# Performance work log

Measured on AMD Instinct MI355X. Metric: run time of the kernel, lower is better.

## Reference

```python
import jax, jax.numpy as jnp
import numpy as np

B, C, H, W = 2, 128, 64, 64


def setup_inputs() -> dict:
    key = jax.random.key(0)
    ks = jax.random.split(key, 16)
    s = 1.0 / np.sqrt(C)
    d = {
        "x": jax.random.normal(ks[0], (B, C, H, W), jnp.float32),
        "y": jax.random.normal(ks[1], (B, C, H, W), jnp.float32),
    }
    names = ["qr", "qi", "kr", "ki", "vr", "vi"]
    for i, n in enumerate(names):
        d["W" + n] = jax.random.normal(ks[2 + 2 * i], (C, C), jnp.float32) * s
        d["b" + n] = jax.random.normal(ks[3 + 2 * i], (C,), jnp.float32) * s
    return d


def _lin(t, Wt, bt):
    # t: [b, n, c]; torch Linear: t @ W^T + b
    return jnp.einsum("bnc,dc->bnd", t, Wt) + bt


def reference(x, y, Wqr, bqr, Wqi, bqi, Wkr, bkr, Wki, bki, Wvr, bvr, Wvi, bvi):
    b, c, h, w = x.shape
    xf = jnp.fft.fft2(x)  # over last two axes (h, w)
    yf = jnp.fft.fft2(y)
    # b c h w -> b (h w) c
    def flat(t):
        return t.transpose(0, 2, 3, 1).reshape(b, h * w, c)
    xr, xi = flat(xf.real), flat(xf.imag)
    yr, yi = flat(yf.real), flat(yf.imag)

    Qr = _lin(xr, Wqr, bqr) - _lin(xi, Wqi, bqi)
    Qi = _lin(xi, Wqr, bqr) + _lin(xr, Wqi, bqi)
    Kr = _lin(yr, Wkr, bkr) - _lin(yi, Wki, bki)
    Ki = _lin(yi, Wkr, bkr) + _lin(yr, Wki, bki)
    Vr = _lin(yr, Wvr, bvr) - _lin(yi, Wvi, bvi)
    Vi = _lin(yi, Wvr, bvr) + _lin(yr, Wvi, bvi)

    sr = jnp.einsum("bnc,bmc->bnm", Qr, Kr) - jnp.einsum("bnc,bmc->bnm", Qi, Ki)
    si = jnp.einsum("bnc,bmc->bnm", Qr, Ki) + jnp.einsum("bnc,bmc->bnm", Qi, Kr)
    scores = jnp.sqrt(sr * sr + si * si + 1e-8)
    attn = jax.nn.softmax(scores, axis=-1)

    out_r = jnp.einsum("bnm,bmc->bnc", attn, Vr)
    out_i = jnp.einsum("bnm,bmc->bnc", attn, Vi)
    out_c = jax.lax.complex(out_r, out_i)
    # b (h w) c -> b c h w
    out_c = out_c.reshape(b, h, w, c).transpose(0, 3, 1, 2)
    return jnp.fft.ifft2(out_c).real
```

## Files before the change

kernel.cpp:

```cpp
#include <hip/hip_runtime.h>
#include <math.h>


#define PI2 6.283185307179586f

typedef __attribute__((ext_vector_type(8))) short short8;
typedef __attribute__((ext_vector_type(4))) float f32x4;

#define MFMA16(A,B,C) __builtin_amdgcn_mfma_f32_16x16x32_bf16((A),(B),(C),0,0,0)

__device__ inline unsigned short f2bf(float x){
  union{float f; unsigned int u;} a; a.f = x;
  unsigned int r = (a.u + 0x7fffu + ((a.u>>16)&1u)) >> 16;
  return (unsigned short)r;
}
__device__ inline float bf2f(unsigned short h){
  union{unsigned int u; float f;} a; a.u = ((unsigned int)h)<<16; return a.f;
}
__device__ inline short8 neg8(short8 x){
  union{short8 v; unsigned int u[4];} a; a.v = x;
  a.u[0]^=0x80008000u; a.u[1]^=0x80008000u; a.u[2]^=0x80008000u; a.u[3]^=0x80008000u;
  return a.v;
}
__device__ inline void gload_lds16(const void* g, void* lds){
  __builtin_amdgcn_global_load_lds((const __attribute__((address_space(1))) unsigned int*)g,
                                   (__attribute__((address_space(3))) unsigned int*)lds,
                                   16, 0, 0);
}

__global__ __launch_bounds__(256) void dft2_fwd_kernel(
    const float* __restrict__ x, const float* __restrict__ y,
    float* __restrict__ xr, float* __restrict__ xi,
    float* __restrict__ yr, float* __restrict__ yi)
{
  __shared__ float Xs[4096];
  __shared__ float Tr[4096], Ti[4096];
  __shared__ float twc[64], tws[64];
  int blk = blockIdx.x;
  const float* src; float *outr, *outi;
  int plane;
  if (blk < 256) { src = x; outr = xr; outi = xi; plane = blk; }
  else           { src = y; outr = yr; outi = yi; plane = blk - 256; }
  int b = plane >> 7, c = plane & 127;
  int t = threadIdx.x;
  if (t < 64) {
    float ang = -PI2 * (float)t / 64.0f;
    twc[t] = cosf(ang); tws[t] = sinf(ang);
  }
  const float* p = src + ((size_t)plane << 12);
  for (int i = t; i < 4096; i += 256) Xs[i] = p[i];
  __syncthreads();
  for (int j = 0; j < 16; j++) {
    int o = t + 256 * j; int h = o >> 6, wp = o & 63;
    float ar = 0.f, ai = 0.f;
    for (int w = 0; w < 64; w++) {
      int k = (w * wp) & 63;
      float v = Xs[h * 64 + w];
      ar = fmaf(v, twc[k], ar);
      ai = fmaf(v, tws[k], ai);
    }
    Tr[h * 64 + wp] = ar; Ti[h * 64 + wp] = ai;
  }
  __syncthreads();
  size_t ob = ((size_t)b * 4096) * 128 + c;
  for (int j = 0; j < 16; j++) {
    int o = t + 256 * j; int hp = o >> 6, wp = o & 63;
    float ar = 0.f, ai = 0.f;
    for (int h = 0; h < 64; h++) {
      int k = (h * hp) & 63;
      float cr = twc[k], ci = tws[k];
      float tr = Tr[h * 64 + wp], ti = Ti[h * 64 + wp];
      ar += tr * cr - ti * ci;
      ai += tr * ci + ti * cr;
    }
    int n = (hp << 6) + wp;
    outr[ob + (size_t)n * 128] = ar;
    outi[ob + (size_t)n * 128] = ai;
  }
}

__global__ __launch_bounds__(256) void proj_kernel(
    const float* __restrict__ xr, const float* __restrict__ xi,
    const float* __restrict__ yr, const float* __restrict__ yi,
    const float* __restrict__ Wqr, const float* __restrict__ bqr,
    const float* __restrict__ Wqi, const float* __restrict__ bqi,
    const float* __restrict__ Wkr, const float* __restrict__ bkr,
    const float* __restrict__ Wki, const float* __restrict__ bki,
    const float* __restrict__ Wvr, const float* __restrict__ bvr,
    const float* __restrict__ Wvi, const float* __restrict__ bvi,
    unsigned short* __restrict__ FQ, unsigned short* __restrict__ FK,
    unsigned short* __restrict__ FV)
{
  __shared__ float Asr[64 * 33], Asi[64 * 33], Wsr[128 * 33], Wsi[128 * 33];
  int nt = blockIdx.x, lin = blockIdx.y, b = blockIdx.z;
  const float *ar, *ai, *Wr, *Wi, *br_, *bi_;
  unsigned short* F;
  if (lin == 0)      { ar = xr; ai = xi; Wr = Wqr; Wi = Wqi; br_ = bqr; bi_ = bqi; F = FQ; }
  else if (lin == 1) { ar = yr; ai = yi; Wr = Wkr; Wi = Wki; br_ = bkr; bi_ = bki; F = FK; }
  else               { ar = yr; ai = yi; Wr = Wvr; Wi = Wvi; br_ = bvr; bi_ = bvi; F = FV; }
  int t = threadIdx.x; int td = t & 15, tn = t >> 4;
  int n0 = nt * 64;
  size_t abase = (size_t)b * 4096 * 128 + (size_t)n0 * 128;
  const size_t PS = (size_t)2 * 4096 * 128;
  float accr[4][8] = {}, acci[4][8] = {};
  for (int kk = 0; kk < 4; kk++) {
    __syncthreads();
    for (int idx = t; idx < 64 * 32; idx += 256) {
      int r = idx >> 5, ccol = idx & 31;
      Asr[r * 33 + ccol] = ar[abase + (size_t)r * 128 + kk * 32 + ccol];
      Asi[r * 33 + ccol] = ai[abase + (size_t)r * 128 + kk * 32 + ccol];
    }
    for (int idx = t; idx < 128 * 32; idx += 256) {
      int r = idx >> 5, ccol = idx & 31;
      Wsr[r * 33 + ccol] = Wr[(size_t)r * 128 + kk * 32 + ccol];
      Wsi[r * 33 + ccol] = Wi[(size_t)r * 128 + kk * 32 + ccol];
    }
    __syncthreads();
    for (int k = 0; k < 32; k++) {
      float a_r[4], a_i[4], w_r[8], w_i[8];
      #pragma unroll
      for (int i = 0; i < 4; i++) {
        a_r[i] = Asr[(tn * 4 + i) * 33 + k];
        a_i[i] = Asi[(tn * 4 + i) * 33 + k];
      }
      #pragma unroll
      for (int jj = 0; jj < 8; jj++) {
        w_r[jj] = Wsr[(td + 16 * jj) * 33 + k];
        w_i[jj] = Wsi[(td + 16 * jj) * 33 + k];
      }
      #pragma unroll
      for (int i = 0; i < 4; i++)
        #pragma unroll
        for (int jj = 0; jj < 8; jj++) {
          accr[i][jj] += a_r[i] * w_r[jj] - a_i[i] * w_i[jj];
          acci[i][jj] += a_i[i] * w_r[jj] + a_r[i] * w_i[jj];
        }
    }
  }
  for (int jj = 0; jj < 8; jj++) {
    int d = td + 16 * jj;
    float brd = br_[d], bid = bi_[d];
    #pragma unroll
    for (int i = 0; i < 4; i++) {
      int n = n0 + tn * 4 + i;
      float cr = accr[i][jj] + (brd - bid);
      float ci = acci[i][jj] + (brd + bid);
      size_t base = ((size_t)b * 4096 + n) * 128 + d;
      if (lin <= 1) {
        unsigned short rh = f2bf(cr); unsigned short rl = f2bf(cr - bf2f(rh));
        unsigned short ih = f2bf(ci); unsigned short il = f2bf(ci - bf2f(ih));
        F[0 * PS + base] = rh;
        F[1 * PS + base] = rl;
        F[2 * PS + base] = ih;
        F[3 * PS + base] = il;
      } else {
        F[0 * PS + base] = f2bf(cr);
        F[1 * PS + base] = f2bf(ci);
      }
    }
  }
}

__global__ __launch_bounds__(256) void qpack_kernel(
    const unsigned short* __restrict__ F, unsigned short* __restrict__ Qpk)
{
  int blk = blockIdx.x;
  int b = blk >> 8, tq = blk & 255;
  int t = threadIdx.x;
  #pragma unroll
  for (int k = 0; k < 4; k++) {
    int idx = t + 256 * k;
    int l = idx & 63, s = (idx >> 6) & 3, a = idx >> 8;
    int n = tq * 16 + (l & 15);
    int c0 = 32 * s + 8 * (l >> 4);
    const short8 v = *(const short8*)(F + (((size_t)(a * 2 + b) * 4096 + n) * 128 + c0));
    *(short8*)(Qpk + (((size_t)((b * 256 + tq) * 16 + a * 4 + s)) * 64 + l) * 8) = v;
  }
}

__global__ __launch_bounds__(256) void kpack_kernel(
    const unsigned short* __restrict__ F, unsigned short* __restrict__ Kpk)
{
  int blk = blockIdx.x;
  int b = blk >> 6, mt = blk & 63;
  int t = threadIdx.x;
  size_t obase = (size_t)blk * 4096;
  #pragma unroll
  for (int k = 0; k < 16; k++) {
    int idx = t + 256 * k;
    int l = idx & 63, s = (idx >> 6) & 3, tml = (idx >> 8) & 3, a = idx >> 10;
    int n = mt * 64 + tml * 16 + (l & 15);
    int c0 = 32 * s + 8 * (l >> 4);
    const short8 v = *(const short8*)(F + (((size_t)(a * 2 + b) * 4096 + n) * 128 + c0));
    *(short8*)(Kpk + (obase + idx) * 8) = v;
  }
}

__global__ __launch_bounds__(256) void vpack_kernel(
    const unsigned short* __restrict__ F, unsigned short* __restrict__ Vpk)
{
  __shared__ unsigned short Vs[2 * 32 * 128];
  int blk = blockIdx.x;
  int b = blk >> 7, sm = blk & 127;
  int t = threadIdx.x;
  const size_t PS = (size_t)2 * 4096 * 128;
  #pragma unroll
  for (int p = 0; p < 2; p++) {
    #pragma unroll
    for (int k = 0; k < 2; k++) {
      int idx8 = t + 256 * k;
      int nn = idx8 >> 4, d0 = (idx8 & 15) * 8;
      const short8 v = *(const short8*)(F + p * PS + ((size_t)(b * 4096 + sm * 32 + nn)) * 128 + d0);
      *(short8*)(Vs + (p * 32 + nn) * 128 + d0) = v;
    }
  }
  __syncthreads();
  size_t obase = (size_t)blk * 1024;
  #pragma unroll
  for (int k = 0; k < 4; k++) {
    int idx = t + 256 * k;
    int lv = idx & 63, tc = idx >> 6;
    int vh = tc >> 3;
    int d = (tc & 7) * 16 + (lv & 15);
    int nb = (lv >> 4) * 8;
    short8 v;
    #pragma unroll
    for (int j = 0; j < 8; j++)
      v[j] = (short)Vs[(vh * 32 + nb + j) * 128 + d];
    *(short8*)(Vpk + (obase + idx) * 8) = v;
  }
}

__global__ __launch_bounds__(512, 1) void attn_mfma_kernel(
    const short* __restrict__ Qpk, const short* __restrict__ Kpk,
    const short* __restrict__ Vpk,
    float* __restrict__ Or_, float* __restrict__ Oi_)
{
  __shared__ __align__(16) short Klds[2][32768];
  __shared__ __align__(16) short Pfrag[2 * 16 * 72];
  __shared__ __align__(16) float rmax[2][16][4];
  __shared__ __align__(16) float escs[2][16];

  const int bi = blockIdx.x;
  const int xg = bi & 7;
  const int b = xg >> 2;
  const int qt = (bi >> 3) * 4 + (xg & 3);
  const int t = threadIdx.x;
  const int w = t >> 6, l = t & 63;
  const int qg = w & 1, ms = w >> 1;
  const int g = l >> 4, c = l & 15;

  const short8* Qp8 = (const short8*)Qpk;
  const int tq = qt * 2 + qg;
  short8 Qf[4][4];
  #pragma unroll
  for (int a = 0; a < 4; a++)
    #pragma unroll
    for (int s = 0; s < 4; s++)
      Qf[a][s] = Qp8[((size_t)((b * 256 + tq) * 16 + a * 4 + s)) * 64 + l];

  f32x4 O[4], Oe;
  #pragma unroll
  for (int nt = 0; nt < 4; nt++) O[nt] = (f32x4){0.f, 0.f, 0.f, 0.f};
  Oe = (f32x4){0.f, 0.f, 0.f, 0.f};
  float Mq = -3e38f;
  short8 Vreg[2][4];
  const short b1 = (short)0x3F80;
  const short8 ones = {b1, b1, b1, b1, b1, b1, b1, b1};

  const char* Kg = (const char*)Kpk;
  {
    const char* gsrc = Kg + ((size_t)(b * 64) << 16);
    char* lb = (char*)&Klds[0][0];
    #pragma unroll
    for (int i2 = 0; i2 < 8; i2++) {
      int ch = w + 8 * i2;
      gload_lds16(gsrc + ch * 1024 + l * 16, lb + ch * 1024);
    }
  }
  const short8* Vp8 = (const short8*)Vpk;
  f32x4 s0;

  for (int mt = 0; mt < 64; mt++) {
    const int cur = mt & 1;
    __syncthreads();
    if (mt + 1 < 64) {
      const char* gsrc = Kg + ((size_t)(b * 64 + mt + 1) << 16);
      char* lb = (char*)&Klds[cur ^ 1][0];
      #pragma unroll
      for (int i2 = 0; i2 < 8; i2++) {
        int ch = w + 8 * i2;
        gload_lds16(gsrc + ch * 1024 + l * 16, lb + ch * 1024);
      }
    }
    if (mt > 0) {
      f32x4 ev = *(const f32x4*)&escs[qg][4 * g];
      #pragma unroll
      for (int r = 0; r < 4; r++) {
        #pragma unroll
        for (int nt = 0; nt < 4; nt++) O[nt][r] *= ev[r];
        Oe[r] *= ev[r];
      }
      #pragma unroll
      for (int ks = 0; ks < 2; ks++) {
        short8 Pa = *(const short8*)&Pfrag[(qg * 16 + c) * 72 + 32 * ks + 8 * g];
        #pragma unroll
        for (int nt = 0; nt < 4; nt++)
          O[nt] = MFMA16(Pa, Vreg[ks][nt], O[nt]);
        Oe = MFMA16(Pa, ones, Oe);
      }
    }
    const short8* kb8 = (const short8*)&Klds[cur][0];
    f32x4 sr = (f32x4){0, 0, 0, 0}, si = (f32x4){0, 0, 0, 0};
    #pragma unroll
    for (int s = 0; s < 4; s++) {
      short8 Arh = kb8[((0 * 4 + ms) * 4 + s) * 64 + l];
      short8 Arl = kb8[((1 * 4 + ms) * 4 + s) * 64 + l];
      short8 Aih = kb8[((2 * 4 + ms) * 4 + s) * 64 + l];
      short8 Ail = kb8[((3 * 4 + ms) * 4 + s) * 64 + l];
      short8 nqh = neg8(Qf[2][s]);
      short8 nql = neg8(Qf[3][s]);
      sr = MFMA16(Arh, Qf[0][s], sr);
      si = MFMA16(Arh, Qf[2][s], si);
      sr = MFMA16(Arh, Qf[1][s], sr);
      si = MFMA16(Arh, Qf[3][s], si);
      sr = MFMA16(Arl, Qf[0][s], sr);
      si = MFMA16(Arl, Qf[2][s], si);
      sr = MFMA16(Aih, nqh, sr);
      si = MFMA16(Aih, Qf[0][s], si);
      sr = MFMA16(Aih, nql, sr);
      si = MFMA16(Aih, Qf[1][s], si);
      sr = MFMA16(Ail, nqh, sr);
      si = MFMA16(Ail, Qf[0][s], si);
    }
    float mloc;
    #pragma unroll
    for (int r = 0; r < 4; r++)
      s0[r] = sqrtf(sr[r] * sr[r] + si[r] * si[r] + 1e-8f);
    mloc = fmaxf(fmaxf(s0[0], s0[1]), fmaxf(s0[2], s0[3]));
    mloc = fmaxf(mloc, __shfl_xor(mloc, 16));
    mloc = fmaxf(mloc, __shfl_xor(mloc, 32));
    if (l < 16) rmax[qg][l][ms] = mloc;
    __syncthreads();
    {
      f32x4 rm4 = *(const f32x4*)&rmax[qg][c][0];
      float nmq = fmaxf(fmaxf(rm4[0], rm4[1]), fmaxf(rm4[2], rm4[3]));
      nmq = fmaxf(Mq, nmq);
      float escq = __expf(Mq - nmq);
      Mq = nmq;
      if (ms == 0 && l < 16) escs[qg][l] = escq;
      #pragma unroll
      for (int ks = 0; ks < 2; ks++)
        #pragma unroll
        for (int nt = 0; nt < 4; nt++)
          Vreg[ks][nt] = Vp8[((size_t)((b * 128 + mt * 2 + ks) * 16 + ms * 4 + nt)) * 64 + l];
      f32x4 p;
      #pragma unroll
      for (int r = 0; r < 4; r++) p[r] = __expf(s0[r] - nmq);
      unsigned int w01 = (unsigned int)f2bf(p[0]) | ((unsigned int)f2bf(p[1]) << 16);
      unsigned int w23 = (unsigned int)f2bf(p[2]) | ((unsigned int)f2bf(p[3]) << 16);
      unsigned int* pw = (unsigned int*)&Pfrag[(qg * 16 + c) * 72 + 16 * ms + 4 * g];
      pw[0] = w01; pw[1] = w23;
    }
  }
  __syncthreads();
  {
    f32x4 ev = *(const f32x4*)&escs[qg][4 * g];
    #pragma unroll
    for (int r = 0; r < 4; r++) {
      #pragma unroll
      for (int nt = 0; nt < 4; nt++) O[nt][r] *= ev[r];
      Oe[r] *= ev[r];
    }
    #pragma unroll
    for (int ks = 0; ks < 2; ks++) {
      short8 Pa = *(const short8*)&Pfrag[(qg * 16 + c) * 72 + 32 * ks + 8 * g];
      #pragma unroll
      for (int nt = 0; nt < 4; nt++)
        O[nt] = MFMA16(Pa, Vreg[ks][nt], O[nt]);
      Oe = MFMA16(Pa, ones, Oe);
    }
  }
  const size_t base = (size_t)b * 4096 * 128;
  f32x4 inv;
  #pragma unroll
  for (int r = 0; r < 4; r++) inv[r] = 1.0f / Oe[r];
  #pragma unroll
  for (int nt = 0; nt < 4; nt++) {
    int cc = ms * 64 + nt * 16 + c;
    #pragma unroll
    for (int r = 0; r < 4; r++) {
      int row = qt * 32 + qg * 16 + 4 * g + r;
      float v = O[nt][r] * inv[r];
      if (cc < 128) Or_[base + (size_t)row * 128 + cc] = v;
      else          Oi_[base + (size_t)row * 128 + cc - 128] = v;
    }
  }
}

__global__ __launch_bounds__(256) void idft2_kernel(
    const float* __restrict__ Or_, const float* __restrict__ Oi_,
    float* __restrict__ out)
{
  __shared__ float Ar[4096], Ai[4096], Tr[4096], Ti[4096];
  __shared__ float twc[64], tws[64];
  int plane = blockIdx.x; int b = plane >> 7, c = plane & 127;
  int t = threadIdx.x;
  if (t < 64) {
    float ang = PI2 * (float)t / 64.0f;
    twc[t] = cosf(ang); tws[t] = sinf(ang);
  }
  size_t ibase = (size_t)b * 4096 * 128 + c;
  for (int i = t; i < 4096; i += 256) {
    Ar[i] = Or_[ibase + (size_t)i * 128];
    Ai[i] = Oi_[ibase + (size_t)i * 128];
  }
  __syncthreads();
  for (int j = 0; j < 16; j++) {
    int o = t + 256 * j; int hp = o >> 6, w = o & 63;
    float tr = 0.f, ti = 0.f;
    for (int wp = 0; wp < 64; wp++) {
      int k = (wp * w) & 63;
      float cr = twc[k], ci = tws[k];
      float ar = Ar[hp * 64 + wp], ai = Ai[hp * 64 + wp];
      tr += ar * cr - ai * ci;
      ti += ai * cr + ar * ci;
    }
    Tr[hp * 64 + w] = tr; Ti[hp * 64 + w] = ti;
  }
  __syncthreads();
  size_t obase = ((size_t)plane) << 12;
  for (int j = 0; j < 16; j++) {
    int o = t + 256 * j; int h = o >> 6, w = o & 63;
    float acc = 0.f;
    for (int hp = 0; hp < 64; hp++) {
      int k = (hp * h) & 63;
      acc += Tr[hp * 64 + w] * twc[k] - Ti[hp * 64 + w] * tws[k];
    }
    out[obase + o] = acc * (1.0f / 4096.0f);
  }
}

extern "C" void kernel_launch(void* const* d_in, const int* in_sizes, int n_in,
                              void* d_out, int out_size, void* d_ws, size_t ws_size,
                              hipStream_t stream) {
  const float* x   = (const float*)d_in[0];
  const float* y   = (const float*)d_in[1];
  const float* Wqr = (const float*)d_in[2];  const float* bqr = (const float*)d_in[3];
  const float* Wqi = (const float*)d_in[4];  const float* bqi = (const float*)d_in[5];
  const float* Wkr = (const float*)d_in[6];  const float* bkr = (const float*)d_in[7];
  const float* Wki = (const float*)d_in[8];  const float* bki = (const float*)d_in[9];
  const float* Wvr = (const float*)d_in[10]; const float* bvr = (const float*)d_in[11];
  const float* Wvi = (const float*)d_in[12]; const float* bvi = (const float*)d_in[13];
  char* wsb = (char*)d_ws;
  if (ws_size < ((size_t)40 << 20)) return;
  unsigned short* FQ  = (unsigned short*)(wsb);
  unsigned short* FK  = (unsigned short*)(wsb + ((size_t)8  << 20));
  unsigned short* FV  = (unsigned short*)(wsb + ((size_t)16 << 20));
  float* xr = (float*)(wsb + ((size_t)20 << 20));
  float* xi = (float*)(wsb + ((size_t)24 << 20));
  float* yr = (float*)(wsb + ((size_t)28 << 20));
  float* yi = (float*)(wsb + ((size_t)32 << 20));
  unsigned short* Qpk = (unsigned short*)(wsb + ((size_t)20 << 20));
  unsigned short* Kpk = (unsigned short*)(wsb + ((size_t)28 << 20));
  unsigned short* Vpk = (unsigned short*)(wsb + ((size_t)36 << 20));
  float* Or_ = (float*)(wsb);
  float* Oi_ = (float*)(wsb + ((size_t)4 << 20));
  float* out = (float*)d_out;

  hipLaunchKernelGGL(dft2_fwd_kernel, dim3(512), dim3(256), 0, stream,
                     x, y, xr, xi, yr, yi);
  hipLaunchKernelGGL(proj_kernel, dim3(64, 3, 2), dim3(256), 0, stream,
                     xr, xi, yr, yi,
                     Wqr, bqr, Wqi, bqi, Wkr, bkr, Wki, bki, Wvr, bvr, Wvi, bvi,
                     FQ, FK, FV);
  hipLaunchKernelGGL(qpack_kernel, dim3(512), dim3(256), 0, stream, FQ, Qpk);
  hipLaunchKernelGGL(kpack_kernel, dim3(128), dim3(256), 0, stream, FK, Kpk);
  hipLaunchKernelGGL(vpack_kernel, dim3(256), dim3(256), 0, stream, FV, Vpk);
  hipLaunchKernelGGL(attn_mfma_kernel, dim3(256), dim3(512), 0, stream,
                     (const short*)Qpk, (const short*)Kpk, (const short*)Vpk, Or_, Oi_);
  hipLaunchKernelGGL(idft2_kernel, dim3(256), dim3(256), 0, stream,
                     Or_, Oi_, out);
}
```

Before: 434.7 us.

## Drop Q/K pack kernels, load from projection layout with swizzled LDS and finer barriers

Removes the qpack and kpack kernels. The attention kernel now reads Q fragments directly from the projection output and DMAs K tiles straight from FK into LDS with an XOR swizzle to avoid bank conflicts. The main loop is unrolled by two over named ping-pong buffers, and __syncthreads is replaced with explicit waitcnt/s_barrier pairs, the vmcnt(8) wait intended to keep the next tile's DMA in flight. It also adds s_setprio around the MFMA section. This cuts two launches and a round trip through global memory, at the cost of strided global reads and hand-tuned synchronisation that could be fragile.

```diff
diff --git a/kernel.cpp b/kernel.cpp
--- a/kernel.cpp
+++ b/kernel.cpp
@@ -161,41 +161,6 @@
   }
 }
 
-__global__ __launch_bounds__(256) void qpack_kernel(
-    const unsigned short* __restrict__ F, unsigned short* __restrict__ Qpk)
-{
-  int blk = blockIdx.x;
-  int b = blk >> 8, tq = blk & 255;
-  int t = threadIdx.x;
-  #pragma unroll
-  for (int k = 0; k < 4; k++) {
-    int idx = t + 256 * k;
-    int l = idx & 63, s = (idx >> 6) & 3, a = idx >> 8;
-    int n = tq * 16 + (l & 15);
-    int c0 = 32 * s + 8 * (l >> 4);
-    const short8 v = *(const short8*)(F + (((size_t)(a * 2 + b) * 4096 + n) * 128 + c0));
-    *(short8*)(Qpk + (((size_t)((b * 256 + tq) * 16 + a * 4 + s)) * 64 + l) * 8) = v;
-  }
-}
-
-__global__ __launch_bounds__(256) void kpack_kernel(
-    const unsigned short* __restrict__ F, unsigned short* __restrict__ Kpk)
-{
-  int blk = blockIdx.x;
-  int b = blk >> 6, mt = blk & 63;
-  int t = threadIdx.x;
-  size_t obase = (size_t)blk * 4096;
-  #pragma unroll
-  for (int k = 0; k < 16; k++) {
-    int idx = t + 256 * k;
-    int l = idx & 63, s = (idx >> 6) & 3, tml = (idx >> 8) & 3, a = idx >> 10;
-    int n = mt * 64 + tml * 16 + (l & 15);
-    int c0 = 32 * s + 8 * (l >> 4);
-    const short8 v = *(const short8*)(F + (((size_t)(a * 2 + b) * 4096 + n) * 128 + c0));
-    *(short8*)(Kpk + (obase + idx) * 8) = v;
-  }
-}
-
 __global__ __launch_bounds__(256) void vpack_kernel(
     const unsigned short* __restrict__ F, unsigned short* __restrict__ Vpk)
 {
@@ -232,11 +197,12 @@
 }
 
 __global__ __launch_bounds__(512, 1) void attn_mfma_kernel(
-    const short* __restrict__ Qpk, const short* __restrict__ Kpk,
+    const unsigned short* __restrict__ FQ, const unsigned short* __restrict__ FK,
     const short* __restrict__ Vpk,
     float* __restrict__ Or_, float* __restrict__ Oi_)
 {
-  __shared__ __align__(16) short Klds[2][32768];
+  __shared__ __align__(16) short K0lds[32768];
+  __shared__ __align__(16) short K1lds[32768];
   __shared__ __align__(16) short Pfrag[2 * 16 * 72];
   __shared__ __align__(16) float rmax[2][16][4];
   __shared__ __align__(16) float escs[2][16];
@@ -250,14 +216,13 @@
   const int qg = w & 1, ms = w >> 1;
   const int g = l >> 4, c = l & 15;
 
-  const short8* Qp8 = (const short8*)Qpk;
   const int tq = qt * 2 + qg;
   short8 Qf[4][4];
   #pragma unroll
   for (int a = 0; a < 4; a++)
     #pragma unroll
     for (int s = 0; s < 4; s++)
-      Qf[a][s] = Qp8[((size_t)((b * 256 + tq) * 16 + a * 4 + s)) * 64 + l];
+      Qf[a][s] = *(const short8*)(FQ + (((size_t)((a * 2 + b) * 4096) + tq * 16 + c) * 128 + 32 * s + 8 * g));
 
   f32x4 O[4], Oe;
   #pragma unroll
@@ -267,32 +232,35 @@
   short8 Vreg[2][4];
   const short b1 = (short)0x3F80;
   const short8 ones = {b1, b1, b1, b1, b1, b1, b1, b1};
-
-  const char* Kg = (const char*)Kpk;
+  const short8* Vp8 = (const short8*)Vpk;
+
   {
-    const char* gsrc = Kg + ((size_t)(b * 64) << 16);
-    char* lb = (char*)&Klds[0][0];
     #pragma unroll
     for (int i2 = 0; i2 < 8; i2++) {
       int ch = w + 8 * i2;
-      gload_lds16(gsrc + ch * 1024 + l * 16, lb + ch * 1024);
-    }
-  }
-  const short8* Vp8 = (const short8*)Vpk;
-  f32x4 s0;
-
-  for (int mt = 0; mt < 64; mt++) {
-    const int cur = mt & 1;
-    __syncthreads();
+      int a = ch >> 4, rr = ((ch & 15) << 2) + g;
+      int u = c ^ (rr & 7);
+      gload_lds16(FK + (((size_t)((a * 2 + b) * 4096) + rr) * 128 + u * 8),
+                  K0lds + (size_t)ch * 512);
+    }
+    asm volatile("s_waitcnt vmcnt(0)" ::: "memory");
+    __builtin_amdgcn_s_barrier();
+    __builtin_amdgcn_sched_barrier(0);
+  }
+
+  auto STEP = [&](const short* kb, short* dmadst, int mt) {
     if (mt + 1 < 64) {
-      const char* gsrc = Kg + ((size_t)(b * 64 + mt + 1) << 16);
-      char* lb = (char*)&Klds[cur ^ 1][0];
+      int m0 = (mt + 1) * 64;
       #pragma unroll
       for (int i2 = 0; i2 < 8; i2++) {
         int ch = w + 8 * i2;
-        gload_lds16(gsrc + ch * 1024 + l * 16, lb + ch * 1024);
-      }
-    }
+        int a = ch >> 4, rr = ((ch & 15) << 2) + g;
+        int u = c ^ (rr & 7);
+        gload_lds16(FK + (((size_t)((a * 2 + b) * 4096) + m0 + rr) * 128 + u * 8),
+                    dmadst + (size_t)ch * 512);
+      }
+    }
+    __builtin_amdgcn_s_setprio(1);
     if (mt > 0) {
       f32x4 ev = *(const f32x4*)&escs[qg][4 * g];
       #pragma unroll
@@ -310,14 +278,15 @@
         Oe = MFMA16(Pa, ones, Oe);
       }
     }
-    const short8* kb8 = (const short8*)&Klds[cur][0];
+    const short8* kb8 = (const short8*)kb;
     f32x4 sr = (f32x4){0, 0, 0, 0}, si = (f32x4){0, 0, 0, 0};
     #pragma unroll
     for (int s = 0; s < 4; s++) {
-      short8 Arh = kb8[((0 * 4 + ms) * 4 + s) * 64 + l];
-      short8 Arl = kb8[((1 * 4 + ms) * 4 + s) * 64 + l];
-      short8 Aih = kb8[((2 * 4 + ms) * 4 + s) * 64 + l];
-      short8 Ail = kb8[((3 * 4 + ms) * 4 + s) * 64 + l];
+      int base0 = (ms * 16 + c) * 16 + ((s * 4 + g) ^ (c & 7));
+      short8 Arh = kb8[base0];
+      short8 Arl = kb8[base0 + 1024];
+      short8 Aih = kb8[base0 + 2048];
+      short8 Ail = kb8[base0 + 3072];
       short8 nqh = neg8(Qf[2][s]);
       short8 nql = neg8(Qf[3][s]);
       sr = MFMA16(Arh, Qf[0][s], sr);
@@ -333,15 +302,18 @@
       sr = MFMA16(Ail, nqh, sr);
       si = MFMA16(Ail, Qf[0][s], si);
     }
-    float mloc;
+    __builtin_amdgcn_s_setprio(0);
+    f32x4 s0;
     #pragma unroll
     for (int r = 0; r < 4; r++)
       s0[r] = sqrtf(sr[r] * sr[r] + si[r] * si[r] + 1e-8f);
-    mloc = fmaxf(fmaxf(s0[0], s0[1]), fmaxf(s0[2], s0[3]));
+    float mloc = fmaxf(fmaxf(s0[0], s0[1]), fmaxf(s0[2], s0[3]));
     mloc = fmaxf(mloc, __shfl_xor(mloc, 16));
     mloc = fmaxf(mloc, __shfl_xor(mloc, 32));
     if (l < 16) rmax[qg][l][ms] = mloc;
-    __syncthreads();
+    asm volatile("s_waitcnt lgkmcnt(0)" ::: "memory");
+    __builtin_amdgcn_s_barrier();
+    __builtin_amdgcn_sched_barrier(0);
     {
       f32x4 rm4 = *(const f32x4*)&rmax[qg][c][0];
       float nmq = fmaxf(fmaxf(rm4[0], rm4[1]), fmaxf(rm4[2], rm4[3]));
@@ -362,8 +334,15 @@
       unsigned int* pw = (unsigned int*)&Pfrag[(qg * 16 + c) * 72 + 16 * ms + 4 * g];
       pw[0] = w01; pw[1] = w23;
     }
-  }
-  __syncthreads();
+    asm volatile("s_waitcnt vmcnt(8) lgkmcnt(0)" ::: "memory");
+    __builtin_amdgcn_s_barrier();
+    __builtin_amdgcn_sched_barrier(0);
+  };
+
+  for (int mt = 0; mt < 64; mt += 2) {
+    STEP(K0lds, K1lds, mt);
+    STEP(K1lds, K0lds, mt + 1);
+  }
   {
     f32x4 ev = *(const f32x4*)&escs[qg][4 * g];
     #pragma unroll
@@ -461,11 +440,9 @@
   float* xi = (float*)(wsb + ((size_t)24 << 20));
   float* yr = (float*)(wsb + ((size_t)28 << 20));
   float* yi = (float*)(wsb + ((size_t)32 << 20));
-  unsigned short* Qpk = (unsigned short*)(wsb + ((size_t)20 << 20));
-  unsigned short* Kpk = (unsigned short*)(wsb + ((size_t)28 << 20));
   unsigned short* Vpk = (unsigned short*)(wsb + ((size_t)36 << 20));
-  float* Or_ = (float*)(wsb);
-  float* Oi_ = (float*)(wsb + ((size_t)4 << 20));
+  float* Or_ = (float*)(wsb + ((size_t)20 << 20));
+  float* Oi_ = (float*)(wsb + ((size_t)24 << 20));
   float* out = (float*)d_out;
 
   hipLaunchKernelGGL(dft2_fwd_kernel, dim3(512), dim3(256), 0, stream,
@@ -474,11 +451,9 @@
                      xr, xi, yr, yi,
                      Wqr, bqr, Wqi, bqi, Wkr, bkr, Wki, bki, Wvr, bvr, Wvi, bvi,
                      FQ, FK, FV);
-  hipLaunchKernelGGL(qpack_kernel, dim3(512), dim3(256), 0, stream, FQ, Qpk);
-  hipLaunchKernelGGL(kpack_kernel, dim3(128), dim3(256), 0, stream, FK, Kpk);
   hipLaunchKernelGGL(vpack_kernel, dim3(256), dim3(256), 0, stream, FV, Vpk);
   hipLaunchKernelGGL(attn_mfma_kernel, dim3(256), dim3(512), 0, stream,
-                     (const short*)Qpk, (const short*)Kpk, (const short*)Vpk, Or_, Oi_);
+                     FQ, FK, (const short*)Vpk, Or_, Oi_);
   hipLaunchKernelGGL(idft2_kernel, dim3(256), dim3(256), 0, stream,
                      Or_, Oi_, out);
 }
```

New measurement: 431.0 us. No clear change (-0.9%).

## Restructure attention kernel with per-wave online softmax and split-K merge

Applied to the files above, without the earlier changes.

Drops the qpack kernel, so the attention kernel loads Q fragments straight from the projection output. The attention loop now handles two K tiles per iteration. Each wave keeps its own running max and its own private P buffer, which removes the cross-wave row-max exchange and one barrier per tile. Each wave accumulates all 256 output columns over its own key slice, and the four partial results are merged at the end through LDS using rescaled max and sum values. This adds register pressure from 16 accumulator and 16 V fragments, a serialized LDS reduction at the end, and s_setprio hints around the MFMA blocks.

```diff
diff --git a/kernel.cpp b/kernel.cpp
--- a/kernel.cpp
+++ b/kernel.cpp
@@ -161,23 +161,6 @@
   }
 }
 
-__global__ __launch_bounds__(256) void qpack_kernel(
-    const unsigned short* __restrict__ F, unsigned short* __restrict__ Qpk)
-{
-  int blk = blockIdx.x;
-  int b = blk >> 8, tq = blk & 255;
-  int t = threadIdx.x;
-  #pragma unroll
-  for (int k = 0; k < 4; k++) {
-    int idx = t + 256 * k;
-    int l = idx & 63, s = (idx >> 6) & 3, a = idx >> 8;
-    int n = tq * 16 + (l & 15);
-    int c0 = 32 * s + 8 * (l >> 4);
-    const short8 v = *(const short8*)(F + (((size_t)(a * 2 + b) * 4096 + n) * 128 + c0));
-    *(short8*)(Qpk + (((size_t)((b * 256 + tq) * 16 + a * 4 + s)) * 64 + l) * 8) = v;
-  }
-}
-
 __global__ __launch_bounds__(256) void kpack_kernel(
     const unsigned short* __restrict__ F, unsigned short* __restrict__ Kpk)
 {
@@ -232,14 +215,16 @@
 }
 
 __global__ __launch_bounds__(512, 1) void attn_mfma_kernel(
-    const short* __restrict__ Qpk, const short* __restrict__ Kpk,
+    const unsigned short* __restrict__ FQ, const short* __restrict__ Kpk,
     const short* __restrict__ Vpk,
     float* __restrict__ Or_, float* __restrict__ Oi_)
 {
-  __shared__ __align__(16) short Klds[2][32768];
-  __shared__ __align__(16) short Pfrag[2 * 16 * 72];
-  __shared__ __align__(16) float rmax[2][16][4];
-  __shared__ __align__(16) float escs[2][16];
+  __shared__ __align__(16) char smem[131072];
+  __shared__ __align__(16) short Ppriv[8][16 * 40];
+  __shared__ float Msh[2][4][16];
+  __shared__ float Lsh[2][4][16];
+  short* K0 = (short*)smem;
+  short* K1 = (short*)(smem + 65536);
 
   const int bi = blockIdx.x;
   const int xg = bi & 7;
@@ -250,68 +235,38 @@
   const int qg = w & 1, ms = w >> 1;
   const int g = l >> 4, c = l & 15;
 
-  const short8* Qp8 = (const short8*)Qpk;
+  const size_t PS = (size_t)2 * 4096 * 128;
   const int tq = qt * 2 + qg;
   short8 Qf[4][4];
   #pragma unroll
   for (int a = 0; a < 4; a++)
     #pragma unroll
     for (int s = 0; s < 4; s++)
-      Qf[a][s] = Qp8[((size_t)((b * 256 + tq) * 16 + a * 4 + s)) * 64 + l];
-
-  f32x4 O[4], Oe;
-  #pragma unroll
-  for (int nt = 0; nt < 4; nt++) O[nt] = (f32x4){0.f, 0.f, 0.f, 0.f};
+      Qf[a][s] = *(const short8*)(FQ + (size_t)a * PS +
+                 ((size_t)(b * 4096) + tq * 16 + c) * 128 + 32 * s + 8 * g);
+
+  f32x4 O[16], Oe;
+  #pragma unroll
+  for (int ntt = 0; ntt < 16; ntt++) O[ntt] = (f32x4){0.f, 0.f, 0.f, 0.f};
   Oe = (f32x4){0.f, 0.f, 0.f, 0.f};
   float Mq = -3e38f;
-  short8 Vreg[2][4];
   const short b1 = (short)0x3F80;
   const short8 ones = {b1, b1, b1, b1, b1, b1, b1, b1};
-
-  const char* Kg = (const char*)Kpk;
-  {
-    const char* gsrc = Kg + ((size_t)(b * 64) << 16);
-    char* lb = (char*)&Klds[0][0];
+  const short8* Vp8 = (const short8*)Vpk;
+
+  auto STAGE = [&](int tile, short* dst) {
+    const char* gsrc = (const char*)Kpk + ((size_t)(b * 64 + tile) << 16);
     #pragma unroll
     for (int i2 = 0; i2 < 8; i2++) {
       int ch = w + 8 * i2;
-      gload_lds16(gsrc + ch * 1024 + l * 16, lb + ch * 1024);
-    }
-  }
-  const short8* Vp8 = (const short8*)Vpk;
-  f32x4 s0;
-
-  for (int mt = 0; mt < 64; mt++) {
-    const int cur = mt & 1;
-    __syncthreads();
-    if (mt + 1 < 64) {
-      const char* gsrc = Kg + ((size_t)(b * 64 + mt + 1) << 16);
-      char* lb = (char*)&Klds[cur ^ 1][0];
-      #pragma unroll
-      for (int i2 = 0; i2 < 8; i2++) {
-        int ch = w + 8 * i2;
-        gload_lds16(gsrc + ch * 1024 + l * 16, lb + ch * 1024);
-      }
-    }
-    if (mt > 0) {
-      f32x4 ev = *(const f32x4*)&escs[qg][4 * g];
-      #pragma unroll
-      for (int r = 0; r < 4; r++) {
-        #pragma unroll
-        for (int nt = 0; nt < 4; nt++) O[nt][r] *= ev[r];
-        Oe[r] *= ev[r];
-      }
-      #pragma unroll
-      for (int ks = 0; ks < 2; ks++) {
-        short8 Pa = *(const short8*)&Pfrag[(qg * 16 + c) * 72 + 32 * ks + 8 * g];
-        #pragma unroll
-        for (int nt = 0; nt < 4; nt++)
-          O[nt] = MFMA16(Pa, Vreg[ks][nt], O[nt]);
-        Oe = MFMA16(Pa, ones, Oe);
-      }
-    }
-    const short8* kb8 = (const short8*)&Klds[cur][0];
-    f32x4 sr = (f32x4){0, 0, 0, 0}, si = (f32x4){0, 0, 0, 0};
+      gload_lds16(gsrc + ch * 1024 + l * 16, (char*)dst + ch * 1024);
+    }
+  };
+  auto QK = [&](const short* kb, f32x4& mag) {
+    const short8* kb8 = (const short8*)kb;
+    f32x4 sr0 = (f32x4){0,0,0,0}, sr1 = (f32x4){0,0,0,0};
+    f32x4 si0 = (f32x4){0,0,0,0}, si1 = (f32x4){0,0,0,0};
+    __builtin_amdgcn_s_setprio(1);
     #pragma unroll
     for (int s = 0; s < 4; s++) {
       short8 Arh = kb8[((0 * 4 + ms) * 4 + s) * 64 + l];
@@ -320,6 +275,8 @@
       short8 Ail = kb8[((3 * 4 + ms) * 4 + s) * 64 + l];
       short8 nqh = neg8(Qf[2][s]);
       short8 nql = neg8(Qf[3][s]);
+      f32x4& sr = (s & 2) ? sr1 : sr0;
+      f32x4& si = (s & 2) ? si1 : si0;
       sr = MFMA16(Arh, Qf[0][s], sr);
       si = MFMA16(Arh, Qf[2][s], si);
       sr = MFMA16(Arh, Qf[1][s], sr);
@@ -333,68 +290,111 @@
       sr = MFMA16(Ail, nqh, sr);
       si = MFMA16(Ail, Qf[0][s], si);
     }
-    float mloc;
-    #pragma unroll
-    for (int r = 0; r < 4; r++)
-      s0[r] = sqrtf(sr[r] * sr[r] + si[r] * si[r] + 1e-8f);
-    mloc = fmaxf(fmaxf(s0[0], s0[1]), fmaxf(s0[2], s0[3]));
+    __builtin_amdgcn_s_setprio(0);
+    #pragma unroll
+    for (int r = 0; r < 4; r++) {
+      float a2 = sr0[r] + sr1[r], b2 = si0[r] + si1[r];
+      mag[r] = sqrtf(a2 * a2 + b2 * b2 + 1e-8f);
+    }
+  };
+
+  STAGE(0, K0);
+  __syncthreads();
+
+  short8 VB[16];
+  f32x4 mag0, mag1;
+
+  for (int mt = 0; mt < 64; mt += 2) {
+    STAGE(mt + 1, K1);
+    {
+      int smv = ((g < 2) ? mt : (mt + 1)) * 2 + (ms >> 1);
+      int gg = 2 * (ms & 1) + (g & 1);
+      size_t vb = ((size_t)((b * 128 + smv) * 16)) * 64 + gg * 16 + c;
+      #pragma unroll
+      for (int ntt = 0; ntt < 16; ntt++)
+        VB[ntt] = Vp8[vb + (size_t)ntt * 64];
+    }
+    QK(K0, mag0);
+    __syncthreads();
+    if (mt + 2 < 64) STAGE(mt + 2, K0);
+    QK(K1, mag1);
+    float mloc = fmaxf(fmaxf(fmaxf(mag0[0], mag0[1]), fmaxf(mag0[2], mag0[3])),
+                       fmaxf(fmaxf(mag1[0], mag1[1]), fmaxf(mag1[2], mag1[3])));
     mloc = fmaxf(mloc, __shfl_xor(mloc, 16));
     mloc = fmaxf(mloc, __shfl_xor(mloc, 32));
-    if (l < 16) rmax[qg][l][ms] = mloc;
+    float Mnew = fmaxf(Mq, mloc);
+    float esc = __expf(Mq - Mnew);
+    Mq = Mnew;
+    {
+      f32x4 p0, p1;
+      #pragma unroll
+      for (int r = 0; r < 4; r++) {
+        p0[r] = __expf(mag0[r] - Mnew);
+        p1[r] = __expf(mag1[r] - Mnew);
+      }
+      unsigned int* pw = (unsigned int*)&Ppriv[w][c * 40 + 4 * g];
+      pw[0] = (unsigned int)f2bf(p0[0]) | ((unsigned int)f2bf(p0[1]) << 16);
+      pw[1] = (unsigned int)f2bf(p0[2]) | ((unsigned int)f2bf(p0[3]) << 16);
+      unsigned int* pw2 = (unsigned int*)&Ppriv[w][c * 40 + 16 + 4 * g];
+      pw2[0] = (unsigned int)f2bf(p1[0]) | ((unsigned int)f2bf(p1[1]) << 16);
+      pw2[1] = (unsigned int)f2bf(p1[2]) | ((unsigned int)f2bf(p1[3]) << 16);
+    }
+    f32x4 esc4;
+    #pragma unroll
+    for (int r = 0; r < 4; r++) esc4[r] = __shfl(esc, 4 * g + r);
+    short8 PA = *(const short8*)&Ppriv[w][c * 40 + (g >> 1) * 16 + 8 * (g & 1)];
+    __builtin_amdgcn_s_setprio(1);
+    #pragma unroll
+    for (int ntt = 0; ntt < 16; ntt++) {
+      #pragma unroll
+      for (int r = 0; r < 4; r++) O[ntt][r] *= esc4[r];
+      O[ntt] = MFMA16(PA, VB[ntt], O[ntt]);
+    }
+    #pragma unroll
+    for (int r = 0; r < 4; r++) Oe[r] *= esc4[r];
+    Oe = MFMA16(PA, ones, Oe);
+    __builtin_amdgcn_s_setprio(0);
     __syncthreads();
-    {
-      f32x4 rm4 = *(const f32x4*)&rmax[qg][c][0];
-      float nmq = fmaxf(fmaxf(rm4[0], rm4[1]), fmaxf(rm4[2], rm4[3]));
-      nmq = fmaxf(Mq, nmq);
-      float escq = __expf(Mq - nmq);
-      Mq = nmq;
-      if (ms == 0 && l < 16) escs[qg][l] = escq;
-      #pragma unroll
-      for (int ks = 0; ks < 2; ks++)
+  }
+
+  if (l < 16) Msh[qg][ms][l] = Mq;
+  __syncthreads();
+  float esc_w[4];
+  #pragma unroll
+  for (int r = 0; r < 4; r++) {
+    int q = 4 * g + r;
+    float m0 = Msh[qg][0][q], m1 = Msh[qg][1][q];
+    float m2 = Msh[qg][2][q], m3 = Msh[qg][3][q];
+    float Mstar = fmaxf(fmaxf(m0, m1), fmaxf(m2, m3));
+    esc_w[r] = __expf(Msh[qg][ms][q] - Mstar);
+  }
+  if (c == 0) {
+    #pragma unroll
+    for (int r = 0; r < 4; r++) Lsh[qg][ms][4 * g + r] = Oe[r] * esc_w[r];
+  }
+  float* Oacc = (float*)smem;
+  for (int round = 0; round < 4; round++) {
+    if (ms == round) {
+      #pragma unroll
+      for (int ntt = 0; ntt < 16; ntt++)
         #pragma unroll
-        for (int nt = 0; nt < 4; nt++)
-          Vreg[ks][nt] = Vp8[((size_t)((b * 128 + mt * 2 + ks) * 16 + ms * 4 + nt)) * 64 + l];
-      f32x4 p;
-      #pragma unroll
-      for (int r = 0; r < 4; r++) p[r] = __expf(s0[r] - nmq);
-      unsigned int w01 = (unsigned int)f2bf(p[0]) | ((unsigned int)f2bf(p[1]) << 16);
-      unsigned int w23 = (unsigned int)f2bf(p[2]) | ((unsigned int)f2bf(p[3]) << 16);
-      unsigned int* pw = (unsigned int*)&Pfrag[(qg * 16 + c) * 72 + 16 * ms + 4 * g];
-      pw[0] = w01; pw[1] = w23;
-    }
-  }
-  __syncthreads();
-  {
-    f32x4 ev = *(const f32x4*)&escs[qg][4 * g];
-    #pragma unroll
-    for (int r = 0; r < 4; r++) {
-      #pragma unroll
-      for (int nt = 0; nt < 4; nt++) O[nt][r] *= ev[r];
-      Oe[r] *= ev[r];
-    }
-    #pragma unroll
-    for (int ks = 0; ks < 2; ks++) {
-      short8 Pa = *(const short8*)&Pfrag[(qg * 16 + c) * 72 + 32 * ks + 8 * g];
-      #pragma unroll
-      for (int nt = 0; nt < 4; nt++)
-        O[nt] = MFMA16(Pa, Vreg[ks][nt], O[nt]);
-      Oe = MFMA16(Pa, ones, Oe);
-    }
+        for (int r = 0; r < 4; r++) {
+          int idx = (qg * 16 + 4 * g + r) * 256 + ntt * 16 + c;
+          float v = O[ntt][r] * esc_w[r];
+          if (round == 0) Oacc[idx] = v; else Oacc[idx] += v;
+        }
+    }
+    __syncthreads();
   }
   const size_t base = (size_t)b * 4096 * 128;
-  f32x4 inv;
-  #pragma unroll
-  for (int r = 0; r < 4; r++) inv[r] = 1.0f / Oe[r];
-  #pragma unroll
-  for (int nt = 0; nt < 4; nt++) {
-    int cc = ms * 64 + nt * 16 + c;
-    #pragma unroll
-    for (int r = 0; r < 4; r++) {
-      int row = qt * 32 + qg * 16 + 4 * g + r;
-      float v = O[nt][r] * inv[r];
-      if (cc < 128) Or_[base + (size_t)row * 128 + cc] = v;
-      else          Oi_[base + (size_t)row * 128 + cc - 128] = v;
-    }
+  #pragma unroll
+  for (int q = 0; q < 16; q++) {
+    float Lq = Lsh[qg][0][q] + Lsh[qg][1][q] + Lsh[qg][2][q] + Lsh[qg][3][q];
+    int cc = ms * 64 + l;
+    float v = Oacc[(qg * 16 + q) * 256 + cc] / Lq;
+    int row = qt * 32 + qg * 16 + q;
+    if (cc < 128) Or_[base + (size_t)row * 128 + cc] = v;
+    else          Oi_[base + (size_t)row * 128 + cc - 128] = v;
   }
 }
 
@@ -461,11 +461,10 @@
   float* xi = (float*)(wsb + ((size_t)24 << 20));
   float* yr = (float*)(wsb + ((size_t)28 << 20));
   float* yi = (float*)(wsb + ((size_t)32 << 20));
-  unsigned short* Qpk = (unsigned short*)(wsb + ((size_t)20 << 20));
   unsigned short* Kpk = (unsigned short*)(wsb + ((size_t)28 << 20));
   unsigned short* Vpk = (unsigned short*)(wsb + ((size_t)36 << 20));
-  float* Or_ = (float*)(wsb);
-  float* Oi_ = (float*)(wsb + ((size_t)4 << 20));
+  float* Or_ = (float*)(wsb + ((size_t)20 << 20));
+  float* Oi_ = (float*)(wsb + ((size_t)24 << 20));
   float* out = (float*)d_out;
 
   hipLaunchKernelGGL(dft2_fwd_kernel, dim3(512), dim3(256), 0, stream,
@@ -474,11 +473,10 @@
                      xr, xi, yr, yi,
                      Wqr, bqr, Wqi, bqi, Wkr, bkr, Wki, bki, Wvr, bvr, Wvi, bvi,
                      FQ, FK, FV);
-  hipLaunchKernelGGL(qpack_kernel, dim3(512), dim3(256), 0, stream, FQ, Qpk);
   hipLaunchKernelGGL(kpack_kernel, dim3(128), dim3(256), 0, stream, FK, Kpk);
   hipLaunchKernelGGL(vpack_kernel, dim3(256), dim3(256), 0, stream, FV, Vpk);
   hipLaunchKernelGGL(attn_mfma_kernel, dim3(256), dim3(512), 0, stream,
-                     (const short*)Qpk, (const short*)Kpk, (const short*)Vpk, Or_, Oi_);
+                     FQ, (const short*)Kpk, (const short*)Vpk, Or_, Oi_);
   hipLaunchKernelGGL(idft2_kernel, dim3(256), dim3(256), 0, stream,
                      Or_, Oi_, out);
 }
```

Result: slower. 551.2 us (+26.8%).
